# Optimization experiments

Hardware: AMD Instinct MI355X
Metric: run time of the kernel (lower is better)

Reference implementation:

```python
import jax, jax.numpy as jnp
import numpy as np

B, S, E, H = 2, 2048, 1024, 16
D = E // H  # head_dim = 64


def setup_inputs() -> dict:
    key = jax.random.key(0)
    ks = jax.random.split(key, 11)
    s = 1.0 / np.sqrt(E)
    return {
        "query": jax.random.normal(ks[0], (B, S, E), jnp.float32),
        "key":   jax.random.normal(ks[1], (B, S, E), jnp.float32),
        "value": jax.random.normal(ks[2], (B, S, E), jnp.float32),
        "q_w": jax.random.uniform(ks[3], (E, E), jnp.float32, -s, s),
        "q_b": jax.random.uniform(ks[4], (E,), jnp.float32, -s, s),
        "k_w": jax.random.uniform(ks[5], (E, E), jnp.float32, -s, s),
        "k_b": jax.random.uniform(ks[6], (E,), jnp.float32, -s, s),
        "v_w": jax.random.uniform(ks[7], (E, E), jnp.float32, -s, s),
        "v_b": jax.random.uniform(ks[8], (E,), jnp.float32, -s, s),
        "o_w": jax.random.uniform(ks[9], (E, E), jnp.float32, -s, s),
        "o_b": jax.random.uniform(ks[10], (E,), jnp.float32, -s, s),
    }


def reference(query, key, value, q_w, q_b, k_w, k_b, v_w, v_b, o_w, o_b):
    b, sq, _ = query.shape
    sk = key.shape[1]
    # linear projections (torch Linear: x @ W.T + b)
    Q = (query @ q_w.T + q_b).reshape(b, sq, H, D).transpose(0, 2, 1, 3)  # b h sq d
    K = (key   @ k_w.T + k_b).reshape(b, sk, H, D).transpose(0, 2, 1, 3)
    V = (value @ v_w.T + v_b).reshape(b, sk, H, D).transpose(0, 2, 1, 3)
    scores = jnp.einsum("bhqd,bhkd->bhqk", Q, K) / jnp.sqrt(jnp.float32(D))
    attn = jax.nn.softmax(scores, axis=-1)
    out = jnp.einsum("bhqk,bhkd->bhqd", attn, V)  # b h sq d
    out = out.transpose(0, 2, 1, 3).reshape(b, sq, E)
    return out @ o_w.T + o_b
```

## Files before the change

kernel.cpp:

```cpp
#include <hip/hip_runtime.h>
#include <stdint.h>

typedef __bf16 bf16x8 __attribute__((ext_vector_type(8)));
typedef short short8 __attribute__((ext_vector_type(8)));
typedef float f32x4 __attribute__((ext_vector_type(4)));
typedef float f32x16 __attribute__((ext_vector_type(16)));
typedef unsigned short u16;
typedef unsigned int u32;

#define MROWS 4096
#define EDIM  1024
#define SQ    2048
#define DH    64

#if __has_builtin(__builtin_amdgcn_exp2f)
#define EXP2(x) __builtin_amdgcn_exp2f(x)
#else
#define EXP2(x) exp2f(x)
#endif

__device__ __forceinline__ u16 f2bf(float f) {
  unsigned u = __builtin_bit_cast(unsigned, f);
  return (u16)((u + 0x7FFFu + ((u >> 16) & 1u)) >> 16);
}

__device__ __forceinline__ u32 cvtpk_bf16(float lo, float hi) {
  u32 r;
  asm("v_cvt_pk_bf16_f32 %0, %1, %2" : "=v"(r) : "v"(lo), "v"(hi));
  return r;
}
__device__ __forceinline__ void swap32(u32& a, u32& b) {
  asm("v_permlane32_swap_b32 %0, %1" : "+v"(a), "+v"(b));
}

__global__ __launch_bounds__(256) void cvt7_kernel(
    const float* __restrict__ s0, const float* __restrict__ s1,
    const float* __restrict__ s2, const float* __restrict__ s3,
    const float* __restrict__ s4, const float* __restrict__ s5,
    const float* __restrict__ s6,
    u16* __restrict__ d0, u16* __restrict__ d1, u16* __restrict__ d2,
    u16* __restrict__ d3, u16* __restrict__ d4, u16* __restrict__ d5,
    u16* __restrict__ d6, int nact, int nw) {
  const float* s; u16* d; int n;
  switch (blockIdx.y) {
    case 0: s = s0; d = d0; n = nact; break;
    case 1: s = s1; d = d1; n = nact; break;
    case 2: s = s2; d = d2; n = nact; break;
    case 3: s = s3; d = d3; n = nw; break;
    case 4: s = s4; d = d4; n = nw; break;
    case 5: s = s5; d = d5; n = nw; break;
    default: s = s6; d = d6; n = nw; break;
  }
  int i = (blockIdx.x * 256 + threadIdx.x) * 8;
  if (i >= n) return;
  float4 a = *(const float4*)(s + i);
  float4 b = *(const float4*)(s + i + 4);
  short8 r;
  r[0] = (short)f2bf(a.x); r[1] = (short)f2bf(a.y);
  r[2] = (short)f2bf(a.z); r[3] = (short)f2bf(a.w);
  r[4] = (short)f2bf(b.x); r[5] = (short)f2bf(b.y);
  r[6] = (short)f2bf(b.z); r[7] = (short)f2bf(b.w);
  *(short8*)(d + i) = r;
}

template <int OUT_F32>
__device__ __forceinline__ void gemm_core(
    const u16* __restrict__ A, const u16* __restrict__ W,
    const float* __restrict__ bias, void* __restrict__ C,
    int m0, int n0, u16* As, u16* Bs) {
  const int tid = threadIdx.x, lane = tid & 63, w = tid >> 6;
  const int r = lane & 15, g = lane >> 4;
  const int wr = w >> 1, wc = w & 1;
  f32x4 acc[4][4] = {};

  for (int kt = 0; kt < 32; ++kt) {
    const int k0 = kt * 32;
    __syncthreads();
#pragma unroll
    for (int i = 0; i < 2; ++i) {
      int c = i * 256 + tid;
      int row = c >> 2, ko = (c & 3) * 8;
      __builtin_amdgcn_global_load_lds(
          (const __attribute__((address_space(1))) void*)(A + (size_t)(m0 + row) * EDIM + k0 + ko),
          (__attribute__((address_space(3))) void*)(As + (i * 256 + w * 64) * 8), 16, 0, 0);
      __builtin_amdgcn_global_load_lds(
          (const __attribute__((address_space(1))) void*)(W + (size_t)(n0 + row) * EDIM + k0 + ko),
          (__attribute__((address_space(3))) void*)(Bs + (i * 256 + w * 64) * 8), 16, 0, 0);
    }
    __syncthreads();
    bf16x8 af[4], bfv[4];
#pragma unroll
    for (int i = 0; i < 4; ++i) {
      af[i]  = *(const bf16x8*)&As[(wr * 64 + i * 16 + r) * 32 + g * 8];
      bfv[i] = *(const bf16x8*)&Bs[(wc * 64 + i * 16 + r) * 32 + g * 8];
    }
#pragma unroll
    for (int mi = 0; mi < 4; ++mi)
#pragma unroll
      for (int ni = 0; ni < 4; ++ni)
        acc[mi][ni] = __builtin_amdgcn_mfma_f32_16x16x32_bf16(af[mi], bfv[ni], acc[mi][ni], 0, 0, 0);
  }
#pragma unroll
  for (int ni = 0; ni < 4; ++ni) {
    const int col = n0 + wc * 64 + ni * 16 + r;
    const float bv = bias[col];
#pragma unroll
    for (int mi = 0; mi < 4; ++mi) {
#pragma unroll
      for (int rr = 0; rr < 4; ++rr) {
        const int rowm = m0 + wr * 64 + mi * 16 + g * 4 + rr;
        float v = acc[mi][ni][rr] + bv;
        if (OUT_F32) ((float*)C)[(size_t)rowm * EDIM + col] = v;
        else ((u16*)C)[(size_t)rowm * EDIM + col] = f2bf(v);
      }
    }
  }
}

__global__ __launch_bounds__(256) void gemm_qkv(
    const u16* __restrict__ X0, const u16* __restrict__ X1, const u16* __restrict__ X2,
    const u16* __restrict__ W0, const u16* __restrict__ W1, const u16* __restrict__ W2,
    const float* __restrict__ b0, const float* __restrict__ b1, const float* __restrict__ b2,
    u16* __restrict__ C0, u16* __restrict__ C1, u16* __restrict__ C2) {
  __shared__ u16 As[128 * 32];
  __shared__ u16 Bs[128 * 32];
  const u16 *A, *W; const float* bias; u16* C;
  switch (blockIdx.z) {
    case 0: A = X0; W = W0; bias = b0; C = C0; break;
    case 1: A = X1; W = W1; bias = b1; C = C1; break;
    default: A = X2; W = W2; bias = b2; C = C2; break;
  }
  gemm_core<0>(A, W, bias, C, blockIdx.y * 128, blockIdx.x * 128, As, Bs);
}

__global__ __launch_bounds__(256) void gemm_oproj(
    const u16* __restrict__ A, const u16* __restrict__ W,
    const float* __restrict__ bias, float* __restrict__ C) {
  __shared__ __align__(16) u16 As[128 * 32];
  __shared__ __align__(16) u16 Bs[64 * 32];
  const int tid = threadIdx.x, lane = tid & 63, w = tid >> 6;
  const int r = lane & 15, g = lane >> 4;
  const int m0 = blockIdx.y * 128, n0 = blockIdx.x * 64;
  const int wr = w >> 1, wc = w & 1;
  f32x4 acc[4][2] = {};

  for (int kt = 0; kt < 32; ++kt) {
    const int k0 = kt * 32;
    __syncthreads();
#pragma unroll
    for (int i = 0; i < 2; ++i) {
      const int c = i * 256 + tid;
      const int row = c >> 2, ko = (c & 3) * 8;
      __builtin_amdgcn_global_load_lds(
          (const __attribute__((address_space(1))) void*)(A + (size_t)(m0 + row) * EDIM + k0 + ko),
          (__attribute__((address_space(3))) void*)(As + (i * 256 + w * 64) * 8), 16, 0, 0);
    }
    {
      const int c = tid;
      const int row = c >> 2, ko = (c & 3) * 8;
      __builtin_amdgcn_global_load_lds(
          (const __attribute__((address_space(1))) void*)(W + (size_t)(n0 + row) * EDIM + k0 + ko),
          (__attribute__((address_space(3))) void*)(Bs + (w * 64) * 8), 16, 0, 0);
    }
    __syncthreads();
    bf16x8 af[4], bfv[2];
#pragma unroll
    for (int i = 0; i < 4; ++i)
      af[i] = *(const bf16x8*)&As[(wr * 64 + i * 16 + r) * 32 + g * 8];
#pragma unroll
    for (int i = 0; i < 2; ++i)
      bfv[i] = *(const bf16x8*)&Bs[(wc * 32 + i * 16 + r) * 32 + g * 8];
#pragma unroll
    for (int mi = 0; mi < 4; ++mi)
#pragma unroll
      for (int ni = 0; ni < 2; ++ni)
        acc[mi][ni] = __builtin_amdgcn_mfma_f32_16x16x32_bf16(af[mi], bfv[ni], acc[mi][ni], 0, 0, 0);
  }
#pragma unroll
  for (int ni = 0; ni < 2; ++ni) {
    const int col = n0 + wc * 32 + ni * 16 + r;
    const float bv = bias[col];
#pragma unroll
    for (int mi = 0; mi < 4; ++mi)
#pragma unroll
      for (int rr = 0; rr < 4; ++rr) {
        const int rowm = m0 + wr * 64 + mi * 16 + g * 4 + rr;
        C[(size_t)rowm * EDIM + col] = acc[mi][ni][rr] + bv;
      }
  }
}

__device__ __forceinline__ void k_stage(const u16* __restrict__ Kg, int kt, int tid,
                                        int w, u16* kb) {
#pragma unroll
  for (int ri = 0; ri < 2; ++ri) {
    int idx = ri * 256 + tid, row = idx >> 3, sl = idx & 7;
    __builtin_amdgcn_global_load_lds(
        (const __attribute__((address_space(1))) void*)(
            Kg + (size_t)(kt * 64 + row) * EDIM + ((sl ^ (row & 7)) * 8)),
        (__attribute__((address_space(3))) void*)(kb + (ri * 256 + w * 64) * 8), 16, 0, 0);
  }
}

__device__ __forceinline__ void v_issue(const u16* __restrict__ Vg, int kt, int tid,
                                        u32* vdw) {
  const int vd0 = (tid & 31) * 2, kvc = tid >> 5;
#pragma unroll
  for (int j = 0; j < 8; ++j)
    vdw[j] = *(const u32*)(Vg + (size_t)(kt * 64 + kvc * 8 + j) * EDIM + vd0);
}

__device__ __forceinline__ void v_write(u16* vt, int tid, const u32* vdw) {
  const int vd0 = (tid & 31) * 2, kvc = tid >> 5;
  union { u32 u[4]; short8 s; } lo8, hi8;
#pragma unroll
  for (int i = 0; i < 4; ++i) {
    lo8.u[i] = (vdw[2 * i] & 0xFFFFu) | (vdw[2 * i + 1] << 16);
    hi8.u[i] = (vdw[2 * i] >> 16) | (vdw[2 * i + 1] & 0xFFFF0000u);
  }
  const int sl = kvc ^ (vd0 & 7);
  *(short8*)&vt[vd0 * 64 + sl * 8] = lo8.s;
  *(short8*)&vt[(vd0 + 1) * 64 + (sl ^ 1) * 8] = hi8.s;
}

#define CE_CONST 0.18033688011112042f

__device__ __forceinline__ void qk_step(f32x16 (&st)[2], const u16* kb,
                                        const bf16x8 (&qf)[4], const int (&colA)[4],
                                        int lq) {
  __builtin_amdgcn_s_setprio(1);
#pragma unroll
  for (int t = 0; t < 2; ++t) {
    f32x16 z = {};
#pragma unroll
    for (int f = 0; f < 4; ++f) {
      const bf16x8 ka = *(const bf16x8*)&kb[(t * 32 + lq) * 64 + colA[f]];
      z = __builtin_amdgcn_mfma_f32_32x32x16_bf16(ka, qf[f], z, 0, 0, 0);
    }
    st[t] = z;
  }
  __builtin_amdgcn_s_setprio(0);
}

__device__ __forceinline__ void softmax_pb(f32x16 (&st)[2], float& m, float& l,
                                           f32x16 (&accO)[2], bf16x8 (&pb)[4]) {
  float vm = fmaxf(st[0][0], st[0][1]);
#pragma unroll
  for (int t = 0; t < 2; ++t)
#pragma unroll
    for (int rr = (t == 0 ? 2 : 0); rr < 16; ++rr) vm = fmaxf(vm, st[t][rr]);
  vm = fmaxf(vm, __shfl_xor(vm, 32));
  if (!__all(vm <= m + 8.0f)) {
    const float mn = fmaxf(m, vm);
    const float scl = EXP2((m - mn) * CE_CONST);
    m = mn;
    l *= scl;
#pragma unroll
    for (int dt = 0; dt < 2; ++dt)
#pragma unroll
      for (int rr = 0; rr < 16; ++rr) accO[dt][rr] *= scl;
  }
  const float mc = m * CE_CONST;
  float ts = 0.f;
#pragma unroll
  for (int t = 0; t < 2; ++t)
#pragma unroll
    for (int rr = 0; rr < 16; ++rr) {
      float pv = EXP2(st[t][rr] * CE_CONST - mc);
      st[t][rr] = pv;
      ts += pv;
    }
  ts += __shfl_xor(ts, 32);
  l += ts;
#pragma unroll
  for (int t = 0; t < 2; ++t)
#pragma unroll
    for (int kh = 0; kh < 2; ++kh) {
      const int rb = kh * 8;
      u32 a0 = cvtpk_bf16(st[t][rb + 0], st[t][rb + 1]);
      u32 b0 = cvtpk_bf16(st[t][rb + 4], st[t][rb + 5]);
      swap32(a0, b0);
      u32 a1 = cvtpk_bf16(st[t][rb + 2], st[t][rb + 3]);
      u32 b1 = cvtpk_bf16(st[t][rb + 6], st[t][rb + 7]);
      swap32(a1, b1);
      union { u32 u[4]; bf16x8 v; } pu;
      pu.u[0] = a0; pu.u[1] = a1; pu.u[2] = b0; pu.u[3] = b1;
      pb[t * 2 + kh] = pu.v;
    }
}

__device__ __forceinline__ void pv_step(f32x16 (&accO)[2], const bf16x8 (&pb)[4],
                                        const u16* vt, const int (&colA)[4], int lq) {
  __builtin_amdgcn_s_setprio(1);
#pragma unroll
  for (int dt = 0; dt < 2; ++dt)
#pragma unroll
    for (int ks = 0; ks < 4; ++ks) {
      const bf16x8 va = *(const bf16x8*)&vt[(dt * 32 + lq) * 64 + colA[ks]];
      accO[dt] = __builtin_amdgcn_mfma_f32_32x32x16_bf16(va, pb[ks], accO[dt], 0, 0, 0);
    }
  __builtin_amdgcn_s_setprio(0);
}

__global__ __launch_bounds__(256) void attn2_kernel(
    const u16* __restrict__ Q, const u16* __restrict__ K,
    const u16* __restrict__ V, u16* __restrict__ O) {
  __shared__ __align__(16) u16 KB[2][64 * 64];
  __shared__ __align__(16) u16 VT[3][64 * 64];
  const int tid = threadIdx.x, lane = tid & 63, w = tid >> 6;
  const int lq = lane & 31, hi = lane >> 5;
  const int bid = blockIdx.x;
  const int b2 = (bid & 7) * 64 + (bid >> 3);
  const int qb = b2 & 15, bh = b2 >> 4;
  const int b = bh >> 4, h = bh & 15;
  const u16* Qg = Q + (size_t)b * SQ * EDIM + h * DH;
  const u16* Kg = K + (size_t)b * SQ * EDIM + h * DH;
  const u16* Vg = V + (size_t)b * SQ * EDIM + h * DH;
  const int q0 = qb * 128 + w * 32;

  bf16x8 qf[4];
#pragma unroll
  for (int f = 0; f < 4; ++f)
    qf[f] = *(const bf16x8*)(Qg + (size_t)(q0 + lq) * EDIM + f * 16 + hi * 8);

  const int swz = (lq & 7) << 4;
  int colA[4];
#pragma unroll
  for (int f = 0; f < 4; ++f) colA[f] = ((f * 32 + hi * 16) ^ swz) >> 1;

  f32x16 accO[2] = {};
  f32x16 stA[2], stB[2];
  bf16x8 pb[4];
  float m = -3e38f, l = 0.f;
  u32 vdw[8];

  k_stage(Kg, 0, tid, w, KB[0]);
  v_issue(Vg, 0, tid, vdw);
  v_write(VT[0], tid, vdw);
  __syncthreads();
  k_stage(Kg, 1, tid, w, KB[1]);
  v_issue(Vg, 1, tid, vdw);
  qk_step(stA, KB[0], qf, colA, lq);
  v_write(VT[1], tid, vdw);
  __syncthreads();

#define ATTN_BODY(T, SP, SN)                                                  \
  {                                                                           \
    if ((T) < 31) { k_stage(Kg, (T) + 1, tid, w, KB[((T) + 1) & 1]);          \
                    v_issue(Vg, (T) + 1, tid, vdw); }                         \
    qk_step(SN, KB[(T) & 1], qf, colA, lq);                                   \
    softmax_pb(SP, m, l, accO, pb);                                           \
    pv_step(accO, pb, VT[((T) - 1) % 3], colA, lq);                           \
    if ((T) < 31) v_write(VT[((T) + 1) % 3], tid, vdw);                       \
    __syncthreads();                                                          \
  }

  for (int t = 1; t < 31; t += 2) {
    ATTN_BODY(t, stA, stB);
    ATTN_BODY(t + 1, stB, stA);
  }
  ATTN_BODY(31, stA, stB);
#undef ATTN_BODY

  softmax_pb(stB, m, l, accO, pb);
  pv_step(accO, pb, VT[31 % 3], colA, lq);

  const float rinv = 1.0f / l;
  u16* Ost = (u16*)KB;
#pragma unroll
  for (int dt = 0; dt < 2; ++dt)
#pragma unroll
    for (int rr = 0; rr < 16; ++rr) {
      const int d = dt * 32 + (rr & 3) + 8 * (rr >> 2) + 4 * hi;
      Ost[w * 2048 + lq * 64 + (d ^ ((lq & 7) << 3))] = f2bf(accO[dt][rr] * rinv);
    }
  __syncthreads();
#pragma unroll
  for (int ri = 0; ri < 4; ++ri) {
    const int idx = ri * 256 + tid;
    const int w2 = idx >> 8, q = (idx >> 3) & 31, c = idx & 7;
    short8 o = *(const short8*)&Ost[w2 * 2048 + q * 64 + ((c ^ (q & 7)) * 8)];
    *(short8*)(O + (size_t)(b * SQ + qb * 128 + w2 * 32 + q) * EDIM + h * DH + c * 8) = o;
  }
}

extern "C" void kernel_launch(void* const* d_in, const int* in_sizes, int n_in,
                              void* d_out, int out_size, void* d_ws, size_t ws_size,
                              hipStream_t stream) {
  (void)in_sizes; (void)n_in; (void)out_size; (void)ws_size;
  const float* query = (const float*)d_in[0];
  const float* key   = (const float*)d_in[1];
  const float* value = (const float*)d_in[2];
  const float* q_w = (const float*)d_in[3];
  const float* q_b = (const float*)d_in[4];
  const float* k_w = (const float*)d_in[5];
  const float* k_b = (const float*)d_in[6];
  const float* v_w = (const float*)d_in[7];
  const float* v_b = (const float*)d_in[8];
  const float* o_w = (const float*)d_in[9];
  const float* o_b = (const float*)d_in[10];

  u16* ws = (u16*)d_ws;
  const size_t NX = (size_t)MROWS * EDIM;
  const size_t NW = (size_t)EDIM * EDIM;
  u16* Xq = ws;
  u16* Xk = Xq + NX;
  u16* Xv = Xk + NX;
  u16* Wq = Xv + NX;
  u16* Wk = Wq + NW;
  u16* Wv = Wk + NW;
  u16* Wo = Wv + NW;
  u16* Qp = Wo + NW;
  u16* Kp = Qp + NX;
  u16* Vp = Kp + NX;
  u16* At = Xq;

  cvt7_kernel<<<dim3((int)(NX / 8 / 256), 7), 256, 0, stream>>>(
      query, key, value, q_w, k_w, v_w, o_w,
      Xq, Xk, Xv, Wq, Wk, Wv, Wo, (int)NX, (int)NW);

  gemm_qkv<<<dim3(8, 32, 3), 256, 0, stream>>>(
      Xq, Xk, Xv, Wq, Wk, Wv, q_b, k_b, v_b, Qp, Kp, Vp);

  attn2_kernel<<<512, 256, 0, stream>>>(Qp, Kp, Vp, At);

  gemm_oproj<<<dim3(16, 32), 256, 0, stream>>>(At, Wo, o_b, (float*)d_out);
}
```

Measured before the change: 135.0 us.

## Write V projection transposed and stage V tiles via direct global-to-LDS loads

The QKV GEMM now writes the V projection in transposed layout (head-dim major, tokens contiguous) using 4-element vector stores. The attention kernel loads each V tile with async global_load_lds into the swizzled LDS buffer, the same way K is loaded. This replaces the register-based 32-bit gathers and the in-register transpose before the LDS write. It removes VGPR pressure and VALU work from the attention loop. In exchange the GEMM epilogue does strided transposed stores, each 8 bytes wide.

```diff
diff --git a/kernel.cpp b/kernel.cpp
--- a/kernel.cpp
+++ b/kernel.cpp
@@ -3,6 +3,7 @@
 
 typedef __bf16 bf16x8 __attribute__((ext_vector_type(8)));
 typedef short short8 __attribute__((ext_vector_type(8)));
+typedef short s16x4 __attribute__((ext_vector_type(4)));
 typedef float f32x4 __attribute__((ext_vector_type(4)));
 typedef float f32x16 __attribute__((ext_vector_type(16)));
 typedef unsigned short u16;
@@ -63,10 +64,10 @@
   *(short8*)(d + i) = r;
 }
 
-template <int OUT_F32>
+template <int TRANSV>
 __device__ __forceinline__ void gemm_core(
     const u16* __restrict__ A, const u16* __restrict__ W,
-    const float* __restrict__ bias, void* __restrict__ C,
+    const float* __restrict__ bias, u16* __restrict__ C,
     int m0, int n0, u16* As, u16* Bs) {
   const int tid = threadIdx.x, lane = tid & 63, w = tid >> 6;
   const int r = lane & 15, g = lane >> 4;
@@ -106,12 +107,18 @@
     const float bv = bias[col];
 #pragma unroll
     for (int mi = 0; mi < 4; ++mi) {
-#pragma unroll
-      for (int rr = 0; rr < 4; ++rr) {
-        const int rowm = m0 + wr * 64 + mi * 16 + g * 4 + rr;
-        float v = acc[mi][ni][rr] + bv;
-        if (OUT_F32) ((float*)C)[(size_t)rowm * EDIM + col] = v;
-        else ((u16*)C)[(size_t)rowm * EDIM + col] = f2bf(v);
+      if (TRANSV == 0) {
+#pragma unroll
+        for (int rr = 0; rr < 4; ++rr) {
+          const int rowm = m0 + wr * 64 + mi * 16 + g * 4 + rr;
+          C[(size_t)rowm * EDIM + col] = f2bf(acc[mi][ni][rr] + bv);
+        }
+      } else {
+        const int rowm0 = m0 + wr * 64 + mi * 16 + g * 4;
+        s16x4 s4;
+#pragma unroll
+        for (int rr = 0; rr < 4; ++rr) s4[rr] = (short)f2bf(acc[mi][ni][rr] + bv);
+        *(s16x4*)&C[(size_t)col * MROWS + rowm0] = s4;
       }
     }
   }
@@ -124,13 +131,14 @@
     u16* __restrict__ C0, u16* __restrict__ C1, u16* __restrict__ C2) {
   __shared__ u16 As[128 * 32];
   __shared__ u16 Bs[128 * 32];
-  const u16 *A, *W; const float* bias; u16* C;
-  switch (blockIdx.z) {
-    case 0: A = X0; W = W0; bias = b0; C = C0; break;
-    case 1: A = X1; W = W1; bias = b1; C = C1; break;
-    default: A = X2; W = W2; bias = b2; C = C2; break;
-  }
-  gemm_core<0>(A, W, bias, C, blockIdx.y * 128, blockIdx.x * 128, As, Bs);
+  if (blockIdx.z == 2) {
+    gemm_core<1>(X2, W2, b2, C2, blockIdx.y * 128, blockIdx.x * 128, As, Bs);
+  } else {
+    const u16 *A, *W; const float* bias; u16* C;
+    if (blockIdx.z == 0) { A = X0; W = W0; bias = b0; C = C0; }
+    else                 { A = X1; W = W1; bias = b1; C = C1; }
+    gemm_core<0>(A, W, bias, C, blockIdx.y * 128, blockIdx.x * 128, As, Bs);
+  }
 }
 
 __global__ __launch_bounds__(256) void gemm_oproj(
@@ -202,25 +210,16 @@
   }
 }
 
-__device__ __forceinline__ void v_issue(const u16* __restrict__ Vg, int kt, int tid,
-                                        u32* vdw) {
-  const int vd0 = (tid & 31) * 2, kvc = tid >> 5;
-#pragma unroll
-  for (int j = 0; j < 8; ++j)
-    vdw[j] = *(const u32*)(Vg + (size_t)(kt * 64 + kvc * 8 + j) * EDIM + vd0);
-}
-
-__device__ __forceinline__ void v_write(u16* vt, int tid, const u32* vdw) {
-  const int vd0 = (tid & 31) * 2, kvc = tid >> 5;
-  union { u32 u[4]; short8 s; } lo8, hi8;
-#pragma unroll
-  for (int i = 0; i < 4; ++i) {
-    lo8.u[i] = (vdw[2 * i] & 0xFFFFu) | (vdw[2 * i + 1] << 16);
-    hi8.u[i] = (vdw[2 * i] >> 16) | (vdw[2 * i + 1] & 0xFFFF0000u);
-  }
-  const int sl = kvc ^ (vd0 & 7);
-  *(short8*)&vt[vd0 * 64 + sl * 8] = lo8.s;
-  *(short8*)&vt[(vd0 + 1) * 64 + (sl ^ 1) * 8] = hi8.s;
+__device__ __forceinline__ void v_stage(const u16* __restrict__ VgT, int kt, int tid,
+                                        int w, u16* vt) {
+#pragma unroll
+  for (int ri = 0; ri < 2; ++ri) {
+    int idx = ri * 256 + tid, row = idx >> 3, sl = idx & 7;
+    __builtin_amdgcn_global_load_lds(
+        (const __attribute__((address_space(1))) void*)(
+            VgT + (size_t)row * MROWS + kt * 64 + ((sl ^ (row & 7)) * 8)),
+        (__attribute__((address_space(3))) void*)(vt + (ri * 256 + w * 64) * 8), 16, 0, 0);
+  }
 }
 
 #define CE_CONST 0.18033688011112042f
@@ -315,7 +314,7 @@
   const int b = bh >> 4, h = bh & 15;
   const u16* Qg = Q + (size_t)b * SQ * EDIM + h * DH;
   const u16* Kg = K + (size_t)b * SQ * EDIM + h * DH;
-  const u16* Vg = V + (size_t)b * SQ * EDIM + h * DH;
+  const u16* VgT = V + (size_t)h * 64 * MROWS + (size_t)b * 2048;
   const int q0 = qb * 128 + w * 32;
 
   bf16x8 qf[4];
@@ -332,26 +331,22 @@
   f32x16 stA[2], stB[2];
   bf16x8 pb[4];
   float m = -3e38f, l = 0.f;
-  u32 vdw[8];
 
   k_stage(Kg, 0, tid, w, KB[0]);
-  v_issue(Vg, 0, tid, vdw);
-  v_write(VT[0], tid, vdw);
+  v_stage(VgT, 0, tid, w, VT[0]);
   __syncthreads();
   k_stage(Kg, 1, tid, w, KB[1]);
-  v_issue(Vg, 1, tid, vdw);
+  v_stage(VgT, 1, tid, w, VT[1]);
   qk_step(stA, KB[0], qf, colA, lq);
-  v_write(VT[1], tid, vdw);
   __syncthreads();
 
 #define ATTN_BODY(T, SP, SN)                                                  \
   {                                                                           \
     if ((T) < 31) { k_stage(Kg, (T) + 1, tid, w, KB[((T) + 1) & 1]);          \
-                    v_issue(Vg, (T) + 1, tid, vdw); }                         \
+                    v_stage(VgT, (T) + 1, tid, w, VT[((T) + 1) % 3]); }       \
     qk_step(SN, KB[(T) & 1], qf, colA, lq);                                   \
     softmax_pb(SP, m, l, accO, pb);                                           \
     pv_step(accO, pb, VT[((T) - 1) % 3], colA, lq);                           \
-    if ((T) < 31) v_write(VT[((T) + 1) % 3], tid, vdw);                       \
     __syncthreads();                                                          \
   }
 
```

After: 144.6 us. 1.07x slower.
